# Kernel tuning notes

Measured on AMD Instinct MI355X. Metric: run time of the kernel, lower is better.

## Reference

```python
import jax, jax.numpy as jnp
import numpy as np

NEG = jnp.float32(-1e10)

def setup_inputs() -> dict:
    key = jax.random.key(0)
    k1, k2, k3, k4 = jax.random.split(key, 4)
    B, Ns, Nr, D = 64, 512, 256, 1024
    return {
        "span_embeddings": jax.random.normal(k1, (B, Ns, D), dtype=jnp.float32),
        "image_embeddings": jax.random.normal(k2, (B, Nr, D), dtype=jnp.float32),
        "span_mask": jax.random.randint(k3, (B, Ns), 0, 2).astype(jnp.int32),
        "image_mask": jax.random.randint(k4, (B, Nr), 0, 2).astype(jnp.int32),
    }

def reference(span_embeddings, image_embeddings, span_mask, image_mask):
    # pair mask: (B, Ns, Nr) = image_mask[b, None, r] * span_mask[b, s, None]
    mask = (image_mask[:, None, :] * span_mask[:, :, None]).astype(span_embeddings.dtype)
    # QK^T with multiplicative mask, then custom zero->-1e10 masking
    att = jnp.einsum('bsd,brd->bsr', span_embeddings, image_embeddings) * mask
    att = jnp.where(att != 0, att, NEG)
    # spans attend over ROIs
    w_first = jax.nn.softmax(att, axis=-1) * mask
    att_first = jnp.einsum('bsr,brd->bsd', w_first, image_embeddings)
    score = jnp.mean(jnp.square(span_embeddings - att_first))
    # ROIs attend over spans (score_type='both')
    att_t = jnp.swapaxes(att, 1, 2)            # (B, Nr, Ns)
    w_second = jax.nn.softmax(att_t, axis=-1) * jnp.swapaxes(mask, 1, 2)
    att_second = jnp.einsum('brs,bsd->brd', w_second, span_embeddings)
    score = score + jnp.mean(jnp.square(image_embeddings - att_second))
    return score, att_first, att
```

## Files before the change

### kernel.cpp

```cpp
#include <hip/hip_runtime.h>
#include <hip/hip_bf16.h>
#include <math.h>

#define B_  64
#define NS  512
#define NR  256
#define DD  1024
#define NEGV (-1e10f)

typedef __attribute__((ext_vector_type(4))) float f32x4;
typedef __attribute__((ext_vector_type(8))) short bf16x8;

__device__ __forceinline__ unsigned short f2bf(float x) {
    unsigned u = __builtin_bit_cast(unsigned, x);
    unsigned r = u + 0x7FFFu + ((u >> 16) & 1u);
    return (unsigned short)(r >> 16);
}
__device__ __forceinline__ unsigned pk2(float x, float y) {
    unsigned r;
    asm("v_cvt_pk_bf16_f32 %0, %1, %2" : "=v"(r) : "v"(x), "v"(y));
    return r;
}
__device__ __forceinline__ void pk_hilo(float x, float y, unsigned& h, unsigned& l) {
    h = pk2(x, y);
    const float hx = __builtin_bit_cast(float, h << 16);
    const float hy = __builtin_bit_cast(float, h & 0xFFFF0000u);
    l = pk2(x - hx, y - hy);
}
__device__ __forceinline__ void gload16(const void* g, void* l) {
    __builtin_amdgcn_global_load_lds((const __attribute__((address_space(1))) void*)g,
                                     (__attribute__((address_space(3))) void*)l, 16, 0, 0);
}

__global__ __launch_bounds__(64) void zero_ws(double* ws) {
    if (threadIdx.x == 0) { ws[0] = 0.0; ws[1] = 0.0; }
}

__global__ __launch_bounds__(256) void att_mfma(
    const float* __restrict__ span, const float* __restrict__ image,
    const int* __restrict__ smask, const int* __restrict__ imask,
    float* __restrict__ att, float* __restrict__ rowP, float* __restrict__ colP,
    int doStats) {
    const int b  = blockIdx.z;
    const int s0 = blockIdx.y * 128;
    const int r0 = blockIdx.x * 128;
    __shared__ unsigned short Ah[128][40], Al[128][40], Bh[128][40], Bl[128][40];
    const int tid  = threadIdx.x;
    const int lane = tid & 63;
    const int w    = tid >> 6;
    const int wso  = (w >> 1) * 64;
    const int wro  = (w & 1) * 64;
    const float* Sp = span  + ((size_t)b * NS + s0) * DD;
    const float* Im = image + ((size_t)b * NR + r0) * DD;

    f32x4 acc[4][4];
    #pragma unroll
    for (int i = 0; i < 4; ++i)
        #pragma unroll
        for (int j = 0; j < 4; ++j) acc[i][j] = (f32x4){0.f, 0.f, 0.f, 0.f};

    const int krel = (tid & 7) * 4;
    const int row0 = tid >> 3;
    const int fr   = lane & 15;
    const int fk   = (lane >> 4) * 8;

    for (int k0 = 0; k0 < DD; k0 += 32) {
        #pragma unroll
        for (int p = 0; p < 4; ++p) {
            const int row = row0 + p * 32;
            const float4 a = *reinterpret_cast<const float4*>(Sp + (size_t)row * DD + k0 + krel);
            const float4 c = *reinterpret_cast<const float4*>(Im + (size_t)row * DD + k0 + krel);
            unsigned h0, l0, h1, l1;
            uint2 u;
            pk_hilo(a.x, a.y, h0, l0); pk_hilo(a.z, a.w, h1, l1);
            u.x = h0; u.y = h1; *reinterpret_cast<uint2*>(&Ah[row][krel]) = u;
            u.x = l0; u.y = l1; *reinterpret_cast<uint2*>(&Al[row][krel]) = u;
            pk_hilo(c.x, c.y, h0, l0); pk_hilo(c.z, c.w, h1, l1);
            u.x = h0; u.y = h1; *reinterpret_cast<uint2*>(&Bh[row][krel]) = u;
            u.x = l0; u.y = l1; *reinterpret_cast<uint2*>(&Bl[row][krel]) = u;
        }
        __syncthreads();
        bf16x8 ah[4], al[4], bh[4], bl[4];
        #pragma unroll
        for (int mf = 0; mf < 4; ++mf) {
            ah[mf] = *reinterpret_cast<const bf16x8*>(&Ah[wso + mf * 16 + fr][fk]);
            al[mf] = *reinterpret_cast<const bf16x8*>(&Al[wso + mf * 16 + fr][fk]);
            bh[mf] = *reinterpret_cast<const bf16x8*>(&Bh[wro + mf * 16 + fr][fk]);
            bl[mf] = *reinterpret_cast<const bf16x8*>(&Bl[wro + mf * 16 + fr][fk]);
        }
        #pragma unroll
        for (int mf = 0; mf < 4; ++mf)
            #pragma unroll
            for (int nf = 0; nf < 4; ++nf) {
                acc[mf][nf] = __builtin_amdgcn_mfma_f32_16x16x32_bf16(ah[mf], bh[nf], acc[mf][nf], 0, 0, 0);
                acc[mf][nf] = __builtin_amdgcn_mfma_f32_16x16x32_bf16(ah[mf], bl[nf], acc[mf][nf], 0, 0, 0);
                acc[mf][nf] = __builtin_amdgcn_mfma_f32_16x16x32_bf16(al[mf], bh[nf], acc[mf][nf], 0, 0, 0);
            }
        __syncthreads();
    }

    float* rowLDS = reinterpret_cast<float*>(&Ah[0][0]);
    float* colLDS = rowLDS + 256;
    const int fq = lane >> 4;
    int imv[4];
    #pragma unroll
    for (int nf = 0; nf < 4; ++nf) imv[nf] = imask[b * NR + r0 + wro + nf * 16 + fr];
    float cmax[4] = {-3.4e38f, -3.4e38f, -3.4e38f, -3.4e38f};
    #pragma unroll
    for (int mf = 0; mf < 4; ++mf) {
        #pragma unroll
        for (int i = 0; i < 4; ++i) {
            const int s = s0 + wso + mf * 16 + fq * 4 + i;
            const int sm = smask[b * NS + s];
            float* orow = att + ((size_t)b * NS + s) * NR + r0 + wro;
            float vj[4];
            #pragma unroll
            for (int nf = 0; nf < 4; ++nf) {
                float v = acc[mf][nf][i] * (float)(sm * imv[nf]);
                v = (v != 0.0f) ? v : NEGV;
                orow[nf * 16 + fr] = v;
                vj[nf] = v;
                cmax[nf] = fmaxf(cmax[nf], v);
            }
            if (doStats) {
                float rm = fmaxf(fmaxf(vj[0], vj[1]), fmaxf(vj[2], vj[3]));
                rm = fmaxf(rm, __shfl_xor(rm, 1));
                rm = fmaxf(rm, __shfl_xor(rm, 2));
                rm = fmaxf(rm, __shfl_xor(rm, 4));
                rm = fmaxf(rm, __shfl_xor(rm, 8));
                if (fr == 0) rowLDS[(wso + mf * 16 + fq * 4 + i) * 2 + (w & 1)] = rm;
            }
        }
    }
    if (doStats) {
        #pragma unroll
        for (int nf = 0; nf < 4; ++nf) {
            cmax[nf] = fmaxf(cmax[nf], __shfl_xor(cmax[nf], 16));
            cmax[nf] = fmaxf(cmax[nf], __shfl_xor(cmax[nf], 32));
        }
        if (lane < 16) {
            #pragma unroll
            for (int nf = 0; nf < 4; ++nf)
                colLDS[(wro + nf * 16 + lane) * 2 + (w >> 1)] = cmax[nf];
        }
        __syncthreads();
        if (tid < 128) {
            rowP[((size_t)b * NS + s0 + tid) * 2 + blockIdx.x] =
                fmaxf(rowLDS[tid * 2 + 0], rowLDS[tid * 2 + 1]);
        } else {
            const int c = tid - 128;
            colP[((size_t)b * NR + r0 + c) * 4 + blockIdx.y] =
                fmaxf(colLDS[c * 2 + 0], colLDS[c * 2 + 1]);
        }
    }
}

__global__ __launch_bounds__(256) void combine_max(
    const float* __restrict__ rowP, const float* __restrict__ colP,
    float* __restrict__ m1, float* __restrict__ m2) {
    const int idx = blockIdx.x * 256 + threadIdx.x;
    if (idx < B_ * NS) {
        m1[idx] = fmaxf(rowP[(size_t)idx * 2 + 0], rowP[(size_t)idx * 2 + 1]);
    } else if (idx < B_ * NS + B_ * NR) {
        const int j = idx - B_ * NS;
        m2[j] = fmaxf(fmaxf(colP[(size_t)j * 4 + 0], colP[(size_t)j * 4 + 1]),
                      fmaxf(colP[(size_t)j * 4 + 2], colP[(size_t)j * 4 + 3]));
    }
}

__global__ __launch_bounds__(256) void transpose_swz(
    const float* __restrict__ src, unsigned short* __restrict__ dst, int N) {
    const int b = blockIdx.z, n0 = blockIdx.y * 32, d0 = blockIdx.x * 32;
    __shared__ unsigned short T[32][36];
    const int t = threadIdx.x;
    {
        const int n = t >> 3, dq = (t & 7) * 4;
        const float4 v = *reinterpret_cast<const float4*>(src + ((size_t)b * N + n0 + n) * DD + d0 + dq);
        T[dq + 0][n] = f2bf(v.x); T[dq + 1][n] = f2bf(v.y);
        T[dq + 2][n] = f2bf(v.z); T[dq + 3][n] = f2bf(v.w);
    }
    __syncthreads();
    {
        const int d = t >> 3, nq = (t & 7) * 4;
        const int dg = d0 + d;
        const int base = n0 + nq;
        const int pos = (base & 63) ^ ((dg & 7) << 3);
        const size_t idx = ((size_t)b * DD + dg) * N + (base & ~63) + pos;
        *reinterpret_cast<ushort4*>(dst + idx) = *reinterpret_cast<const ushort4*>(&T[d][nq]);
    }
}

__global__ __launch_bounds__(256) void gemm1_fused(
    const float* __restrict__ att, const unsigned short* __restrict__ imgT,
    const float* __restrict__ span,
    const int* __restrict__ smask, const int* __restrict__ imask,
    const float* __restrict__ m1,
    float* __restrict__ att_first, double* __restrict__ wsum) {
    const int b = blockIdx.z, m0 = blockIdx.y * 64, d0 = blockIdx.x * 256;
    __shared__ unsigned short As[64 * 64];
    __shared__ unsigned short Bs[256 * 64];
    __shared__ float redsum[256];
    __shared__ float m1s[64], sms[64], rowsumS[64];
    __shared__ float ims[256];
    const int tid = threadIdx.x, lane = tid & 63, w = tid >> 6;
    const int fr = lane & 15, fq = lane >> 4;
    if (tid < 64) {
        m1s[tid] = m1[b * NS + m0 + tid];
        sms[tid] = (float)smask[b * NS + m0 + tid];
    }
    ims[tid] = (float)imask[b * NR + tid];
    f32x4 acc[4][4];
    #pragma unroll
    for (int i = 0; i < 4; ++i)
        #pragma unroll
        for (int j = 0; j < 4; ++j) acc[i][j] = (f32x4){0.f, 0.f, 0.f, 0.f};

    const int arow = tid >> 2;
    const int acg  = (tid & 3) * 16;
    const int akey = (arow & 7) << 3;
    const int srow = tid >> 3;
    const int scol = (tid & 7) * 16;
    float rsum = 0.0f;
    __syncthreads();

    for (int kc = 0; kc < NR / 64; ++kc) {
        const char* bsrc = (const char*)(imgT + ((size_t)b * DD + d0) * NR) + kc * 128 + scol;
        #pragma unroll
        for (int c = 0; c < 8; ++c)
            gload16(bsrc + (size_t)(c * 32 + srow) * (NR * 2), (char*)Bs + (c * 256 + tid) * 16);
        {
            const float* ap = att + ((size_t)b * NS + m0 + arow) * NR + kc * 64 + acg;
            const float m1v = m1s[arow];
            const float4 a0 = *reinterpret_cast<const float4*>(ap);
            const float4 a1 = *reinterpret_cast<const float4*>(ap + 4);
            const float4 a2 = *reinterpret_cast<const float4*>(ap + 8);
            const float4 a3 = *reinterpret_cast<const float4*>(ap + 12);
            float e[16];
            e[0] = __expf(a0.x - m1v); e[1] = __expf(a0.y - m1v);
            e[2] = __expf(a0.z - m1v); e[3] = __expf(a0.w - m1v);
            e[4] = __expf(a1.x - m1v); e[5] = __expf(a1.y - m1v);
            e[6] = __expf(a1.z - m1v); e[7] = __expf(a1.w - m1v);
            e[8] = __expf(a2.x - m1v); e[9] = __expf(a2.y - m1v);
            e[10] = __expf(a2.z - m1v); e[11] = __expf(a2.w - m1v);
            e[12] = __expf(a3.x - m1v); e[13] = __expf(a3.y - m1v);
            e[14] = __expf(a3.z - m1v); e[15] = __expf(a3.w - m1v);
            #pragma unroll
            for (int j = 0; j < 16; ++j) rsum += e[j];
            const int ib = kc * 64 + acg;
            uint4 u;
            u.x = pk2(e[0] * ims[ib + 0], e[1] * ims[ib + 1]);
            u.y = pk2(e[2] * ims[ib + 2], e[3] * ims[ib + 3]);
            u.z = pk2(e[4] * ims[ib + 4], e[5] * ims[ib + 5]);
            u.w = pk2(e[6] * ims[ib + 6], e[7] * ims[ib + 7]);
            *reinterpret_cast<uint4*>(&As[arow * 64 + (acg ^ akey)]) = u;
            u.x = pk2(e[8] * ims[ib + 8], e[9] * ims[ib + 9]);
            u.y = pk2(e[10] * ims[ib + 10], e[11] * ims[ib + 11]);
            u.z = pk2(e[12] * ims[ib + 12], e[13] * ims[ib + 13]);
            u.w = pk2(e[14] * ims[ib + 14], e[15] * ims[ib + 15]);
            *reinterpret_cast<uint4*>(&As[arow * 64 + ((acg + 8) ^ akey)]) = u;
        }
        __syncthreads();
        #pragma unroll
        for (int ks = 0; ks < 2; ++ks) {
            bf16x8 aF[4], bF[4];
            #pragma unroll
            for (int mf = 0; mf < 4; ++mf) {
                const int row = mf * 16 + fr;
                const int pos = (ks * 32 + fq * 8) ^ ((row & 7) << 3);
                aF[mf] = *reinterpret_cast<const bf16x8*>(&As[row * 64 + pos]);
            }
            #pragma unroll
            for (int nf = 0; nf < 4; ++nf) {
                const int row = w * 64 + nf * 16 + fr;
                const int pos = (ks * 32 + fq * 8) ^ ((row & 7) << 3);
                bF[nf] = *reinterpret_cast<const bf16x8*>(&Bs[row * 64 + pos]);
            }
            #pragma unroll
            for (int mf = 0; mf < 4; ++mf)
                #pragma unroll
                for (int nf = 0; nf < 4; ++nf)
                    acc[mf][nf] = __builtin_amdgcn_mfma_f32_16x16x32_bf16(aF[mf], bF[nf], acc[mf][nf], 0, 0, 0);
        }
        __syncthreads();
    }
    rsum += __shfl_xor(rsum, 1);
    rsum += __shfl_xor(rsum, 2);
    if ((tid & 3) == 0) rowsumS[arow] = rsum;
    __syncthreads();

    float sumsq = 0.0f;
    #pragma unroll
    for (int mf = 0; mf < 4; ++mf) {
        #pragma unroll
        for (int i = 0; i < 4; ++i) {
            const int row = mf * 16 + fq * 4 + i;
            const float fac = sms[row] / rowsumS[row];
            const size_t base = ((size_t)b * NS + m0 + row) * DD + d0 + w * 64;
            #pragma unroll
            for (int nf = 0; nf < 4; ++nf) {
                const float v = acc[mf][nf][i] * fac;
                const float rv = span[base + nf * 16 + fr];
                att_first[base + nf * 16 + fr] = v;
                const float dx = rv - v;
                sumsq += dx * dx;
            }
        }
    }
    redsum[tid] = sumsq; __syncthreads();
    for (int off = 128; off; off >>= 1) {
        if (tid < off) redsum[tid] += redsum[tid + off];
        __syncthreads();
    }
    if (tid == 0) atomicAdd(wsum, (double)redsum[0]);
}

__global__ __launch_bounds__(256) void gemm2_fused(
    const float* __restrict__ att, const unsigned short* __restrict__ spT,
    const float* __restrict__ image,
    const int* __restrict__ smask, const int* __restrict__ imask,
    const float* __restrict__ m2, double* __restrict__ wsum) {
    const int b = blockIdx.z, r0 = blockIdx.y * 64, d0 = blockIdx.x * 256;
    __shared__ unsigned short As[64 * 64];
    __shared__ unsigned short Bs[256 * 64];
    __shared__ float redsum[256];
    __shared__ float m2s[64], imsv[64], colsumS[64];
    __shared__ float smsK[512];
    __shared__ float cs4[4][64];
    const int tid = threadIdx.x, lane = tid & 63, w = tid >> 6;
    const int fr = lane & 15, fq = lane >> 4;
    if (tid < 64) {
        m2s[tid] = m2[b * NR + r0 + tid];
        imsv[tid] = (float)imask[b * NR + r0 + tid];
    }
    smsK[tid]       = (float)smask[b * NS + tid];
    smsK[tid + 256] = (float)smask[b * NS + 256 + tid];
    f32x4 acc[4][4];
    #pragma unroll
    for (int i = 0; i < 4; ++i)
        #pragma unroll
        for (int j = 0; j < 4; ++j) acc[i][j] = (f32x4){0.f, 0.f, 0.f, 0.f};

    const int asr = tid >> 2;
    const int arg = (tid & 3) * 16;
    const int srow = tid >> 3;
    const int scol = (tid & 7) * 16;
    float csum[16];
    #pragma unroll
    for (int j = 0; j < 16; ++j) csum[j] = 0.0f;
    __syncthreads();

    for (int kc = 0; kc < NS / 64; ++kc) {
        const char* bsrc = (const char*)(spT + ((size_t)b * DD + d0) * NS) + kc * 128 + scol;
        #pragma unroll
        for (int c = 0; c < 8; ++c)
            gload16(bsrc + (size_t)(c * 32 + srow) * (NS * 2), (char*)Bs + (c * 256 + tid) * 16);
        {
            const float* ap = att + ((size_t)b * NS + kc * 64 + asr) * NR + r0 + arg;
            const float smv = smsK[kc * 64 + asr];
            const float4 a0 = *reinterpret_cast<const float4*>(ap);
            const float4 a1 = *reinterpret_cast<const float4*>(ap + 4);
            const float4 a2 = *reinterpret_cast<const float4*>(ap + 8);
            const float4 a3 = *reinterpret_cast<const float4*>(ap + 12);
            const float av[16] = {a0.x, a0.y, a0.z, a0.w, a1.x, a1.y, a1.z, a1.w,
                                  a2.x, a2.y, a2.z, a2.w, a3.x, a3.y, a3.z, a3.w};
            const int slo = asr & 7;
            const int shi = asr >> 3;
            #pragma unroll
            for (int j = 0; j < 16; ++j) {
                const int r = arg + j;
                const float e = __expf(av[j] - m2s[r]);
                csum[j] += e;
                const int pos = slo | ((shi ^ (r & 7)) << 3);
                As[r * 64 + pos] = f2bf(e * smv);
            }
        }
        __syncthreads();
        #pragma unroll
        for (int ks = 0; ks < 2; ++ks) {
            bf16x8 aF[4], bF[4];
            #pragma unroll
            for (int mf = 0; mf < 4; ++mf) {
                const int row = mf * 16 + fr;
                const int pos = (ks * 32 + fq * 8) ^ ((row & 7) << 3);
                aF[mf] = *reinterpret_cast<const bf16x8*>(&As[row * 64 + pos]);
            }
            #pragma unroll
            for (int nf = 0; nf < 4; ++nf) {
                const int row = w * 64 + nf * 16 + fr;
                const int pos = (ks * 32 + fq * 8) ^ ((row & 7) << 3);
                bF[nf] = *reinterpret_cast<const bf16x8*>(&Bs[row * 64 + pos]);
            }
            #pragma unroll
            for (int mf = 0; mf < 4; ++mf)
                #pragma unroll
                for (int nf = 0; nf < 4; ++nf)
                    acc[mf][nf] = __builtin_amdgcn_mfma_f32_16x16x32_bf16(aF[mf], bF[nf], acc[mf][nf], 0, 0, 0);
        }
        __syncthreads();
    }
    #pragma unroll
    for (int j = 0; j < 16; ++j) {
        float v = csum[j];
        v += __shfl_xor(v, 4);
        v += __shfl_xor(v, 8);
        v += __shfl_xor(v, 16);
        v += __shfl_xor(v, 32);
        if (lane < 4) cs4[w][lane * 16 + j] = v;
    }
    __syncthreads();
    if (tid < 64) colsumS[tid] = (cs4[0][tid] + cs4[1][tid]) + (cs4[2][tid] + cs4[3][tid]);
    __syncthreads();

    float sumsq = 0.0f;
    #pragma unroll
    for (int mf = 0; mf < 4; ++mf) {
        #pragma unroll
        for (int i = 0; i < 4; ++i) {
            const int row = mf * 16 + fq * 4 + i;
            const float fac = imsv[row] / colsumS[row];
            const size_t base = ((size_t)b * NR + r0 + row) * DD + d0 + w * 64;
            #pragma unroll
            for (int nf = 0; nf < 4; ++nf) {
                const float dx = image[base + nf * 16 + fr] - acc[mf][nf][i] * fac;
                sumsq += dx * dx;
            }
        }
    }
    redsum[tid] = sumsq; __syncthreads();
    for (int off = 128; off; off >>= 1) {
        if (tid < off) redsum[tid] += redsum[tid + off];
        __syncthreads();
    }
    if (tid == 0) atomicAdd(wsum + 1, (double)redsum[0]);
}

__global__ __launch_bounds__(256) void first_kernel(
    const float* __restrict__ span, const float* __restrict__ image,
    const int* __restrict__ smask, const int* __restrict__ imask,
    const float* __restrict__ att, float* __restrict__ att_first,
    double* __restrict__ ws) {
    const int b  = blockIdx.y;
    const int s0 = blockIdx.x * 32;
    __shared__ float wT[256][36];
    __shared__ float Is[32][132];
    __shared__ float red[256];
    const int tid  = threadIdx.x;
    const int lane = tid & 63, wave = tid >> 6;
    for (int i = 0; i < 8; ++i) {
        const int srel = wave * 8 + i;
        const int s    = s0 + srel;
        const float4 v = *reinterpret_cast<const float4*>(att + ((size_t)b * NS + s) * NR + lane * 4);
        float m = fmaxf(fmaxf(v.x, v.y), fmaxf(v.z, v.w));
        #pragma unroll
        for (int off = 32; off; off >>= 1) m = fmaxf(m, __shfl_xor(m, off));
        float4 e;
        e.x = expf(v.x - m); e.y = expf(v.y - m); e.z = expf(v.z - m); e.w = expf(v.w - m);
        float sum = e.x + e.y + e.z + e.w;
        #pragma unroll
        for (int off = 32; off; off >>= 1) sum += __shfl_xor(sum, off);
        const float fac = (float)smask[b * NS + s] / sum;
        const int4 im4 = *reinterpret_cast<const int4*>(imask + b * NR + lane * 4);
        wT[lane * 4 + 0][srel] = e.x * fac * (float)im4.x;
        wT[lane * 4 + 1][srel] = e.y * fac * (float)im4.y;
        wT[lane * 4 + 2][srel] = e.z * fac * (float)im4.z;
        wT[lane * 4 + 3][srel] = e.w * fac * (float)im4.w;
    }
    __syncthreads();
    float sumsq = 0.0f;
    const int txd = tid & 31;
    const int tys = tid >> 5;
    const float* Ib = image + (size_t)b * NR * DD;
    for (int dc = 0; dc < 8; ++dc) {
        const int d0 = dc * 128;
        float acc[4][4] = {};
        for (int rc = 0; rc < 8; ++rc) {
            const int r0 = rc * 32;
            {
                const int rr = tid >> 3;
                const int cb = tid & 7;
                const float* src = Ib + (size_t)(r0 + rr) * DD + d0;
                #pragma unroll
                for (int q = 0; q < 4; ++q)
                    *reinterpret_cast<float4*>(&Is[rr][(cb + 8 * q) * 4]) =
                        *reinterpret_cast<const float4*>(src + (cb + 8 * q) * 4);
            }
            __syncthreads();
            #pragma unroll 4
            for (int rr = 0; rr < 32; ++rr) {
                const float4 wv = *reinterpret_cast<const float4*>(&wT[r0 + rr][tys * 4]);
                const float4 iv = *reinterpret_cast<const float4*>(&Is[rr][txd * 4]);
                const float wvv[4] = {wv.x, wv.y, wv.z, wv.w};
                const float ivv[4] = {iv.x, iv.y, iv.z, iv.w};
                #pragma unroll
                for (int i = 0; i < 4; ++i)
                    #pragma unroll
                    for (int j = 0; j < 4; ++j)
                        acc[i][j] += wvv[i] * ivv[j];
            }
            __syncthreads();
        }
        #pragma unroll
        for (int i = 0; i < 4; ++i) {
            const int s = s0 + tys * 4 + i;
            const size_t base = ((size_t)b * NS + s) * DD + d0 + txd * 4;
            const float4 af = {acc[i][0], acc[i][1], acc[i][2], acc[i][3]};
            *reinterpret_cast<float4*>(att_first + base) = af;
            const float4 sp = *reinterpret_cast<const float4*>(span + base);
            float dx;
            dx = sp.x - af.x; sumsq += dx * dx;
            dx = sp.y - af.y; sumsq += dx * dx;
            dx = sp.z - af.z; sumsq += dx * dx;
            dx = sp.w - af.w; sumsq += dx * dx;
        }
    }
    red[tid] = sumsq; __syncthreads();
    for (int off = 128; off; off >>= 1) {
        if (tid < off) red[tid] += red[tid + off];
        __syncthreads();
    }
    if (tid == 0) atomicAdd(ws, (double)red[0]);
}

__global__ __launch_bounds__(256) void second_kernel(
    const float* __restrict__ span, const float* __restrict__ image,
    const int* __restrict__ smask, const int* __restrict__ imask,
    const float* __restrict__ att, double* __restrict__ ws) {
    const int b  = blockIdx.y;
    const int r0 = blockIdx.x * 32;
    __shared__ float w2s[32][36];
    __shared__ float Ss[32][132];
    __shared__ float mArr[32], fArr[32];
    __shared__ float redm[8][32];
    __shared__ float red[256];
    const int tid = threadIdx.x;
    const int rr = tid & 31, q = tid >> 5;
    const float* attb = att + (size_t)b * NS * NR + r0 + rr;
    float mloc = -3.4e38f;
    for (int t = 0; t < 64; ++t)
        mloc = fmaxf(mloc, attb[(size_t)(q * 64 + t) * NR]);
    redm[q][rr] = mloc;
    __syncthreads();
    if (tid < 32) {
        float m = redm[0][tid];
        #pragma unroll
        for (int qq = 1; qq < 8; ++qq) m = fmaxf(m, redm[qq][tid]);
        mArr[tid] = m;
    }
    __syncthreads();
    const float mcol = mArr[rr];
    float sloc = 0.0f;
    for (int t = 0; t < 64; ++t)
        sloc += expf(attb[(size_t)(q * 64 + t) * NR] - mcol);
    redm[q][rr] = sloc;
    __syncthreads();
    if (tid < 32) {
        float s = 0.0f;
        #pragma unroll
        for (int qq = 0; qq < 8; ++qq) s += redm[qq][tid];
        fArr[tid] = (float)imask[b * NR + r0 + tid] / s;
    }
    __syncthreads();
    float sumsq = 0.0f;
    const int txd = tid & 31;
    const int tyr = tid >> 5;
    const float* Sb = span + (size_t)b * NS * DD;
    for (int dc = 0; dc < 8; ++dc) {
        const int d0 = dc * 128;
        float acc[4][4] = {};
        for (int sc = 0; sc < 16; ++sc) {
            const int sb0 = sc * 32;
            {
                const int sr = tid >> 3;
                const int cb = tid & 7;
                const float* src = Sb + (size_t)(sb0 + sr) * DD + d0;
                #pragma unroll
                for (int qq = 0; qq < 4; ++qq)
                    *reinterpret_cast<float4*>(&Ss[sr][(cb + 8 * qq) * 4]) =
                        *reinterpret_cast<const float4*>(src + (cb + 8 * qq) * 4);
            }
            {
                const int ss = tid >> 3;
                const int rq = (tid & 7) * 4;
                const int s  = sb0 + ss;
                const float4 v = *reinterpret_cast<const float4*>(att + ((size_t)b * NS + s) * NR + r0 + rq);
                const float smv = (float)smask[b * NS + s];
                float4 wv;
                wv.x = expf(v.x - mArr[rq + 0]) * fArr[rq + 0] * smv;
                wv.y = expf(v.y - mArr[rq + 1]) * fArr[rq + 1] * smv;
                wv.z = expf(v.z - mArr[rq + 2]) * fArr[rq + 2] * smv;
                wv.w = expf(v.w - mArr[rq + 3]) * fArr[rq + 3] * smv;
                *reinterpret_cast<float4*>(&w2s[ss][rq]) = wv;
            }
            __syncthreads();
            #pragma unroll 4
            for (int ss = 0; ss < 32; ++ss) {
                const float4 wv = *reinterpret_cast<const float4*>(&w2s[ss][tyr * 4]);
                const float4 sv = *reinterpret_cast<const float4*>(&Ss[ss][txd * 4]);
                const float wvv[4] = {wv.x, wv.y, wv.z, wv.w};
                const float svv[4] = {sv.x, sv.y, sv.z, sv.w};
                #pragma unroll
                for (int i = 0; i < 4; ++i)
                    #pragma unroll
                    for (int j = 0; j < 4; ++j)
                        acc[i][j] += wvv[i] * svv[j];
            }
            __syncthreads();
        }
        #pragma unroll
        for (int i = 0; i < 4; ++i) {
            const int r = r0 + tyr * 4 + i;
            const float4 iv = *reinterpret_cast<const float4*>(image + ((size_t)b * NR + r) * DD + d0 + txd * 4);
            float dx;
            dx = iv.x - acc[i][0]; sumsq += dx * dx;
            dx = iv.y - acc[i][1]; sumsq += dx * dx;
            dx = iv.z - acc[i][2]; sumsq += dx * dx;
            dx = iv.w - acc[i][3]; sumsq += dx * dx;
        }
    }
    red[tid] = sumsq; __syncthreads();
    for (int off = 128; off; off >>= 1) {
        if (tid < off) red[tid] += red[tid + off];
        __syncthreads();
    }
    if (tid == 0) atomicAdd(ws + 1, (double)red[0]);
}

__global__ __launch_bounds__(64) void score_kernel(const double* __restrict__ ws, float* __restrict__ out) {
    if (threadIdx.x == 0) {
        out[0] = (float)(ws[0] / (double)((size_t)B_ * NS * DD) +
                         ws[1] / (double)((size_t)B_ * NR * DD));
    }
}

extern "C" void kernel_launch(void* const* d_in, const int* in_sizes, int n_in,
                              void* d_out, int out_size, void* d_ws, size_t ws_size,
                              hipStream_t stream) {
    const float* span  = (const float*)d_in[0];
    const float* image = (const float*)d_in[1];
    const int*   smask = (const int*)d_in[2];
    const int*   imask = (const int*)d_in[3];
    float* out       = (float*)d_out;
    float* att_first = out + 1;
    float* att       = out + 1 + (size_t)B_ * NS * DD;

    char* base = (char*)d_ws;
    double* wsum = (double*)base;
    float* m1   = (float*)(base + 512);
    float* m2   = m1 + (size_t)B_ * NS;
    float* rowP = m2 + (size_t)B_ * NR;
    float* colP = rowP + (size_t)B_ * NS * 2;
    char* X0 = (char*)(colP + (size_t)B_ * NR * 4);
    unsigned short* imgT = (unsigned short*)X0;
    unsigned short* spT  = (unsigned short*)X0;
    const size_t NEED = (size_t)(X0 - base) + (size_t)B_ * DD * NS * 2;
    const int wsok = (ws_size >= NEED) ? 1 : 0;

    zero_ws<<<dim3(1), dim3(64), 0, stream>>>(wsum);
    att_mfma<<<dim3(NR / 128, NS / 128, B_), dim3(256), 0, stream>>>(
        span, image, smask, imask, att, rowP, colP, wsok);

    if (wsok) {
        combine_max<<<dim3((B_ * NS + B_ * NR) / 256), dim3(256), 0, stream>>>(
            rowP, colP, m1, m2);
        transpose_swz<<<dim3(DD / 32, NR / 32, B_), dim3(256), 0, stream>>>(image, imgT, NR);
        gemm1_fused<<<dim3(DD / 256, NS / 64, B_), dim3(256), 0, stream>>>(
            att, imgT, span, smask, imask, m1, att_first, wsum);
        transpose_swz<<<dim3(DD / 32, NS / 32, B_), dim3(256), 0, stream>>>(span, spT, NS);
        gemm2_fused<<<dim3(DD / 256, NR / 64, B_), dim3(256), 0, stream>>>(
            att, spT, image, smask, imask, m2, wsum);
    } else {
        first_kernel<<<dim3(NS / 32, B_), dim3(256), 0, stream>>>(span, image, smask, imask, att, att_first, wsum);
        second_kernel<<<dim3(NR / 32, B_), dim3(256), 0, stream>>>(span, image, smask, imask, att, wsum);
    }
    score_kernel<<<dim3(1), dim3(64), 0, stream>>>(wsum, out);
}
```

Baseline: 311.6 us.

## Compute softmax weights once per 32-row block and loop over all D chunks

gemm1_fused now handles 32 span rows per block across the full D dimension, so each block computes exp and packs the full 32x256 probability tile into LDS once. Previously the same exp/pack work was repeated for each of the four D tiles. The image transpose uses a new 32-wide swizzle to match the smaller K-step B tile. In exchange the grid shrinks to 1024 blocks, each looping serially over D with a sync-heavy, unpipelined K loop.

```diff
diff --git a/kernel.cpp b/kernel.cpp
--- a/kernel.cpp
+++ b/kernel.cpp
@@ -168,6 +168,7 @@
     }
 }
 
+template<int MODE>
 __global__ __launch_bounds__(256) void transpose_swz(
     const float* __restrict__ src, unsigned short* __restrict__ dst, int N) {
     const int b = blockIdx.z, n0 = blockIdx.y * 32, d0 = blockIdx.x * 32;
@@ -183,9 +184,14 @@
     {
         const int d = t >> 3, nq = (t & 7) * 4;
         const int dg = d0 + d;
-        const int base = n0 + nq;
-        const int pos = (base & 63) ^ ((dg & 7) << 3);
-        const size_t idx = ((size_t)b * DD + dg) * N + (base & ~63) + pos;
+        const int k = n0 + nq;
+        int pos;
+        if constexpr (MODE == 0) {
+            pos = (k & ~63) + ((k & 63) ^ ((dg & 7) << 3));
+        } else {
+            pos = (k & ~31) + (((((k >> 3) & 3) ^ ((dg >> 1) & 3)) << 3) | (k & 7));
+        }
+        const size_t idx = ((size_t)b * DD + dg) * N + pos;
         *reinterpret_cast<ushort4*>(dst + idx) = *reinterpret_cast<const ushort4*>(&T[d][nq]);
     }
 }
@@ -196,113 +202,105 @@
     const int* __restrict__ smask, const int* __restrict__ imask,
     const float* __restrict__ m1,
     float* __restrict__ att_first, double* __restrict__ wsum) {
-    const int b = blockIdx.z, m0 = blockIdx.y * 64, d0 = blockIdx.x * 256;
-    __shared__ unsigned short As[64 * 64];
-    __shared__ unsigned short Bs[256 * 64];
+    const int id = blockIdx.x;
+    const int b  = id & 63;
+    const int m0 = (id >> 6) * 32;
+    __shared__ unsigned short As[32 * 256];
+    __shared__ unsigned short Bs[256 * 32];
+    __shared__ float ims[256];
+    __shared__ float m1s[32], sms[32], rowsumS[32];
     __shared__ float redsum[256];
-    __shared__ float m1s[64], sms[64], rowsumS[64];
-    __shared__ float ims[256];
     const int tid = threadIdx.x, lane = tid & 63, w = tid >> 6;
     const int fr = lane & 15, fq = lane >> 4;
-    if (tid < 64) {
+    ims[tid] = (float)imask[b * NR + tid];
+    if (tid < 32) {
         m1s[tid] = m1[b * NS + m0 + tid];
         sms[tid] = (float)smask[b * NS + m0 + tid];
     }
-    ims[tid] = (float)imask[b * NR + tid];
-    f32x4 acc[4][4];
-    #pragma unroll
-    for (int i = 0; i < 4; ++i)
-        #pragma unroll
-        for (int j = 0; j < 4; ++j) acc[i][j] = (f32x4){0.f, 0.f, 0.f, 0.f};
-
-    const int arow = tid >> 2;
-    const int acg  = (tid & 3) * 16;
-    const int akey = (arow & 7) << 3;
-    const int srow = tid >> 3;
-    const int scol = (tid & 7) * 16;
-    float rsum = 0.0f;
-    __syncthreads();
-
-    for (int kc = 0; kc < NR / 64; ++kc) {
-        const char* bsrc = (const char*)(imgT + ((size_t)b * DD + d0) * NR) + kc * 128 + scol;
-        #pragma unroll
-        for (int c = 0; c < 8; ++c)
-            gload16(bsrc + (size_t)(c * 32 + srow) * (NR * 2), (char*)Bs + (c * 256 + tid) * 16);
-        {
-            const float* ap = att + ((size_t)b * NS + m0 + arow) * NR + kc * 64 + acg;
-            const float m1v = m1s[arow];
-            const float4 a0 = *reinterpret_cast<const float4*>(ap);
-            const float4 a1 = *reinterpret_cast<const float4*>(ap + 4);
-            const float4 a2 = *reinterpret_cast<const float4*>(ap + 8);
-            const float4 a3 = *reinterpret_cast<const float4*>(ap + 12);
-            float e[16];
-            e[0] = __expf(a0.x - m1v); e[1] = __expf(a0.y - m1v);
-            e[2] = __expf(a0.z - m1v); e[3] = __expf(a0.w - m1v);
-            e[4] = __expf(a1.x - m1v); e[5] = __expf(a1.y - m1v);
-            e[6] = __expf(a1.z - m1v); e[7] = __expf(a1.w - m1v);
-            e[8] = __expf(a2.x - m1v); e[9] = __expf(a2.y - m1v);
-            e[10] = __expf(a2.z - m1v); e[11] = __expf(a2.w - m1v);
-            e[12] = __expf(a3.x - m1v); e[13] = __expf(a3.y - m1v);
-            e[14] = __expf(a3.z - m1v); e[15] = __expf(a3.w - m1v);
-            #pragma unroll
-            for (int j = 0; j < 16; ++j) rsum += e[j];
-            const int ib = kc * 64 + acg;
+    __syncthreads();
+
+    const int arow = tid >> 3, cg = tid & 7;
+    {
+        const float* ap = att + ((size_t)b * NS + m0 + arow) * NR + cg * 32;
+        const float m1v = m1s[arow];
+        float rsum = 0.0f;
+        #pragma unroll
+        for (int gg = 0; gg < 4; ++gg) {
+            const float4 a0 = *reinterpret_cast<const float4*>(ap + gg * 8);
+            const float4 a1 = *reinterpret_cast<const float4*>(ap + gg * 8 + 4);
+            const float e0 = __expf(a0.x - m1v), e1 = __expf(a0.y - m1v);
+            const float e2 = __expf(a0.z - m1v), e3 = __expf(a0.w - m1v);
+            const float e4 = __expf(a1.x - m1v), e5 = __expf(a1.y - m1v);
+            const float e6 = __expf(a1.z - m1v), e7 = __expf(a1.w - m1v);
+            rsum += (e0 + e1 + e2 + e3) + (e4 + e5 + e6 + e7);
+            const int kb = cg * 32 + gg * 8;
             uint4 u;
-            u.x = pk2(e[0] * ims[ib + 0], e[1] * ims[ib + 1]);
-            u.y = pk2(e[2] * ims[ib + 2], e[3] * ims[ib + 3]);
-            u.z = pk2(e[4] * ims[ib + 4], e[5] * ims[ib + 5]);
-            u.w = pk2(e[6] * ims[ib + 6], e[7] * ims[ib + 7]);
-            *reinterpret_cast<uint4*>(&As[arow * 64 + (acg ^ akey)]) = u;
-            u.x = pk2(e[8] * ims[ib + 8], e[9] * ims[ib + 9]);
-            u.y = pk2(e[10] * ims[ib + 10], e[11] * ims[ib + 11]);
-            u.z = pk2(e[12] * ims[ib + 12], e[13] * ims[ib + 13]);
-            u.w = pk2(e[14] * ims[ib + 14], e[15] * ims[ib + 15]);
-            *reinterpret_cast<uint4*>(&As[arow * 64 + ((acg + 8) ^ akey)]) = u;
-        }
-        __syncthreads();
-        #pragma unroll
-        for (int ks = 0; ks < 2; ++ks) {
-            bf16x8 aF[4], bF[4];
-            #pragma unroll
-            for (int mf = 0; mf < 4; ++mf) {
+            u.x = pk2(e0 * ims[kb + 0], e1 * ims[kb + 1]);
+            u.y = pk2(e2 * ims[kb + 2], e3 * ims[kb + 3]);
+            u.z = pk2(e4 * ims[kb + 4], e5 * ims[kb + 5]);
+            u.w = pk2(e6 * ims[kb + 6], e7 * ims[kb + 7]);
+            const int g = cg * 4 + gg;
+            *reinterpret_cast<uint4*>(&As[arow * 256 + ((g ^ (arow & 7)) << 3)]) = u;
+        }
+        rsum += __shfl_xor(rsum, 1);
+        rsum += __shfl_xor(rsum, 2);
+        rsum += __shfl_xor(rsum, 4);
+        if ((tid & 7) == 0) rowsumS[arow] = rsum;
+    }
+    __syncthreads();
+
+    float sumsq = 0.0f;
+    const int brow = tid >> 2;
+    const int bcol = (tid & 3) * 8;
+    for (int dc = 0; dc < 4; ++dc) {
+        const int d0 = dc * 256;
+        f32x4 acc[2][4];
+        #pragma unroll
+        for (int i = 0; i < 2; ++i)
+            #pragma unroll
+            for (int j = 0; j < 4; ++j) acc[i][j] = (f32x4){0.f, 0.f, 0.f, 0.f};
+        for (int kcc = 0; kcc < 8; ++kcc) {
+            const unsigned short* bsrc = imgT + ((size_t)b * DD + d0) * NR + kcc * 32;
+            #pragma unroll
+            for (int c = 0; c < 4; ++c)
+                gload16(bsrc + (size_t)(c * 64 + brow) * NR + bcol,
+                        (char*)Bs + c * 4096 + tid * 16);
+            __syncthreads();
+            bf16x8 aF[2], bF[4];
+            #pragma unroll
+            for (int mf = 0; mf < 2; ++mf) {
                 const int row = mf * 16 + fr;
-                const int pos = (ks * 32 + fq * 8) ^ ((row & 7) << 3);
-                aF[mf] = *reinterpret_cast<const bf16x8*>(&As[row * 64 + pos]);
+                aF[mf] = *reinterpret_cast<const bf16x8*>(
+                    &As[row * 256 + (((kcc * 4 + fq) ^ (row & 7)) << 3)]);
             }
             #pragma unroll
             for (int nf = 0; nf < 4; ++nf) {
-                const int row = w * 64 + nf * 16 + fr;
-                const int pos = (ks * 32 + fq * 8) ^ ((row & 7) << 3);
-                bF[nf] = *reinterpret_cast<const bf16x8*>(&Bs[row * 64 + pos]);
-            }
-            #pragma unroll
-            for (int mf = 0; mf < 4; ++mf)
+                const int dr = w * 64 + nf * 16 + fr;
+                bF[nf] = *reinterpret_cast<const bf16x8*>(
+                    &Bs[dr * 32 + ((fq ^ ((dr >> 1) & 3)) << 3)]);
+            }
+            #pragma unroll
+            for (int mf = 0; mf < 2; ++mf)
                 #pragma unroll
                 for (int nf = 0; nf < 4; ++nf)
                     acc[mf][nf] = __builtin_amdgcn_mfma_f32_16x16x32_bf16(aF[mf], bF[nf], acc[mf][nf], 0, 0, 0);
-        }
-        __syncthreads();
-    }
-    rsum += __shfl_xor(rsum, 1);
-    rsum += __shfl_xor(rsum, 2);
-    if ((tid & 3) == 0) rowsumS[arow] = rsum;
-    __syncthreads();
-
-    float sumsq = 0.0f;
-    #pragma unroll
-    for (int mf = 0; mf < 4; ++mf) {
-        #pragma unroll
-        for (int i = 0; i < 4; ++i) {
-            const int row = mf * 16 + fq * 4 + i;
-            const float fac = sms[row] / rowsumS[row];
-            const size_t base = ((size_t)b * NS + m0 + row) * DD + d0 + w * 64;
-            #pragma unroll
-            for (int nf = 0; nf < 4; ++nf) {
-                const float v = acc[mf][nf][i] * fac;
-                const float rv = span[base + nf * 16 + fr];
-                att_first[base + nf * 16 + fr] = v;
-                const float dx = rv - v;
-                sumsq += dx * dx;
+            __syncthreads();
+        }
+        #pragma unroll
+        for (int mf = 0; mf < 2; ++mf) {
+            #pragma unroll
+            for (int i = 0; i < 4; ++i) {
+                const int row = mf * 16 + fq * 4 + i;
+                const float fac = sms[row] / rowsumS[row];
+                const size_t base = ((size_t)b * NS + m0 + row) * DD + d0 + w * 64;
+                #pragma unroll
+                for (int nf = 0; nf < 4; ++nf) {
+                    const float v = acc[mf][nf][i] * fac;
+                    const float rv = span[base + nf * 16 + fr];
+                    att_first[base + nf * 16 + fr] = v;
+                    const float dx = rv - v;
+                    sumsq += dx * dx;
+                }
             }
         }
     }
@@ -662,10 +660,10 @@
     if (wsok) {
         combine_max<<<dim3((B_ * NS + B_ * NR) / 256), dim3(256), 0, stream>>>(
             rowP, colP, m1, m2);
-        transpose_swz<<<dim3(DD / 32, NR / 32, B_), dim3(256), 0, stream>>>(image, imgT, NR);
-        gemm1_fused<<<dim3(DD / 256, NS / 64, B_), dim3(256), 0, stream>>>(
+        transpose_swz<1><<<dim3(DD / 32, NR / 32, B_), dim3(256), 0, stream>>>(image, imgT, NR);
+        gemm1_fused<<<dim3((NS / 32) * B_), dim3(256), 0, stream>>>(
             att, imgT, span, smask, imask, m1, att_first, wsum);
-        transpose_swz<<<dim3(DD / 32, NS / 32, B_), dim3(256), 0, stream>>>(span, spT, NS);
+        transpose_swz<0><<<dim3(DD / 32, NS / 32, B_), dim3(256), 0, stream>>>(span, spT, NS);
         gemm2_fused<<<dim3(DD / 256, NR / 64, B_), dim3(256), 0, stream>>>(
             att, spT, image, smask, imask, m2, wsum);
     } else {
```

After: 337.6 us. 1.08x slower.
